# Kernel tuning notes

Hardware: AMD Instinct MI355X
Metric: run time of the kernel (lower is better)

The kernel has to match this reference:

```python
import jax, jax.numpy as jnp
import numpy as np

B, N, H = 128, 2048, 128
FEAT = 15


def setup_inputs() -> dict:
    key = jax.random.key(0)
    ks = jax.random.split(key, 24)
    f32 = jnp.float32
    inp = {
        'x':   jax.random.normal(ks[0], (B, N), f32),
        'x1':  jax.random.uniform(ks[1], (B, N), f32),
        'x2':  jax.random.uniform(ks[2], (B, N), f32),
        'z1':  jax.random.uniform(ks[3], (B, N), f32),
        'z2':  jax.random.uniform(ks[4], (B, N), f32),
        'x1E': jax.random.uniform(ks[5], (B, N), f32),
        'x2E': jax.random.uniform(ks[6], (B, N), f32),
        'z1E': jax.random.uniform(ks[7], (B, N), f32),
        'z2E': jax.random.uniform(ks[8], (B, N), f32),
        'muB': jax.random.uniform(ks[9], (B, 1), f32, 0.01, 0.1),
        'lb':  jax.random.normal(ks[10], (B, N), f32) - 2.0,
        'ub':  jax.random.normal(ks[11], (B, N), f32) + 2.0,
        'has_lb': jnp.ones((B, N), bool),
        'has_ub': jnp.ones((B, N), bool),
        # LSTM params (PyTorch gate order i, f, g, o)
        'W_ih': 0.1 * jax.random.normal(ks[12], (4 * H, FEAT), f32),
        'W_hh': 0.1 * jax.random.normal(ks[13], (4 * H, H), f32),
        'b_ih': 0.1 * jax.random.normal(ks[14], (4 * H,), f32),
        'b_hh': 0.1 * jax.random.normal(ks[15], (4 * H,), f32),
        # px_head: Linear(H,H) -> ReLU -> Linear(H,1)
        'W1': 0.1 * jax.random.normal(ks[16], (H, H), f32),
        'b1': 0.1 * jax.random.normal(ks[17], (H,), f32),
        'W2': 0.1 * jax.random.normal(ks[18], (1, H), f32),
        'b2': 0.1 * jax.random.normal(ks[19], (1,), f32),
    }
    return inp


def _forward(x, x1, x2, z1, z2, x1E, x2E, z1E, z2E, muB, lb, ub,
             W_ih, W_hh, b_ih, b_hh, W1, b1, W2, b2, has_lb, has_ub):
    Bb, n = x.shape
    eps = 1e-12
    # slack / bad-coordinate handling
    z1 = jnp.where((z1 + muB) <= 0, 0.0, z1)
    z2 = jnp.where((z2 + muB) <= 0, 0.0, z2)
    # quadratic merit stand-in: M = 0.5(||x||^2 + ||z1||^2 + ||z2||^2)
    grad_x, grad_z1, grad_z2 = x, z1, z2
    invD1 = jnp.clip((z1 + muB) / (x1 + muB + eps), 0.0, 100.0)
    invD2 = jnp.clip((z2 + muB) / (x2 + muB + eps), 0.0, 100.0)
    muB_bn = jnp.broadcast_to(muB, (Bb, n))
    # [B, n, 15] -> [B*n, 15]
    feat = jnp.stack([x, x1, x2, z1, z2, grad_x, grad_z1, grad_z2,
                      x1E, x2E, z1E, z2E, muB_bn, invD1, invD2], axis=-1)
    feat = feat.reshape(Bb * n, FEAT)
    # single-step LSTM cell, h0 = c0 = 0 so W_hh @ h0 vanishes
    gates = feat @ W_ih.T + b_ih + b_hh          # [B*n, 4H]
    i, f, g, o = jnp.split(gates, 4, axis=-1)
    c = jax.nn.sigmoid(i) * jnp.tanh(g)
    h = jax.nn.sigmoid(o) * jnp.tanh(c)          # [B*n, H]
    # MLP head -> per-coordinate positive step size
    p = jax.nn.relu(h @ W1.T + b1) @ W2.T + b2   # [B*n, 1]
    p_x = jnp.abs(p).reshape(Bb, n)
    # elementwise updates
    d_x = -p_x * grad_x
    x_new = x + d_x
    z1 = z1 - invD1 * (-p_x * grad_x + grad_z1)
    z2 = z2 - invD2 * (p_x * grad_x + grad_z2)
    x = x_new  # project_step = identity accept
    x1 = jnp.where(has_lb, x - lb, 0.0)
    x2 = jnp.where(has_ub, ub - x, 0.0)
    return jnp.concatenate([x, x1, x2, z1, z2], axis=-1)  # [B, 5n]


def reference(x, x1, x2, z1, z2, x1E, x2E, z1E, z2E, muB, lb, ub,
              has_lb, has_ub, W_ih, W_hh, b_ih, b_hh, W1, b1, W2, b2):
    return _forward(x, x1, x2, z1, z2, x1E, x2E, z1E, z2E, muB, lb, ub,
                    W_ih, W_hh, b_ih, b_hh, W1, b1, W2, b2, has_lb, has_ub)
```

## Files before the change

### kernel.cpp

```cpp
#include <hip/hip_runtime.h>


typedef _Float16 half8v  __attribute__((ext_vector_type(8)));
typedef _Float16 half4v  __attribute__((ext_vector_type(4)));
typedef float    float4v __attribute__((ext_vector_type(4)));

#define N_SZ   2048
#define ROWS   262144
#define BLOCKT 512
#define NWAVES 8
#define NBLK   512
#define WITERS 2
#define WROWS  32

#define HS 136
#define SS 40

__device__ __forceinline__ float fast_rcp(float x) { return __builtin_amdgcn_rcpf(x); }
__device__ __forceinline__ float sigm(float x)  { return fast_rcp(1.0f + __expf(-x)); }
__device__ __forceinline__ float tanh_f(float x){ return 1.0f - 2.0f * fast_rcp(1.0f + __expf(2.0f * x)); }
__device__ __forceinline__ float tanh_c(float y) {
    const float t = y * y;
    return y * __builtin_fmaf(t, __builtin_fmaf(t, __builtin_fmaf(t,
            -0.02714f, 0.12052f), -0.33157f), 0.99986f);
}

__global__ __launch_bounds__(BLOCKT)
void ps_lstm_hp2(const float* __restrict__ x_,
                 const float* __restrict__ x1_,
                 const float* __restrict__ x2_,
                 const float* __restrict__ z1_,
                 const float* __restrict__ z2_,
                 const float* __restrict__ x1E_,
                 const float* __restrict__ x2E_,
                 const float* __restrict__ z1E_,
                 const float* __restrict__ z2E_,
                 const float* __restrict__ muB_,
                 const float* __restrict__ lb_,
                 const float* __restrict__ ub_,
                 const float* __restrict__ Wih_,
                 const float* __restrict__ bih_,
                 const float* __restrict__ bhh_,
                 const float* __restrict__ W1_,
                 const float* __restrict__ b1_,
                 const float* __restrict__ W2_,
                 const float* __restrict__ b2_,
                 float* __restrict__ out_)
{
    __shared__ __align__(16) _Float16 fragWih[3 * 8 * 64 * 8];
    __shared__ __align__(16) _Float16 sW1T [128 * HS];
    __shared__ __align__(16) _Float16 sFeat[NWAVES][WROWS * 16];
    __shared__ __align__(16) _Float16 sHs  [NWAVES][16 * SS];
    __shared__ float sP[NWAVES][WROWS];

    const int tid  = threadIdx.x;
    const int lane = tid & 63;
    const int w    = tid >> 6;
    const int c    = lane & 15;
    const int q    = lane >> 4;

    for (int ch = tid; ch < 3 * 8 * 64; ch += BLOCKT) {
        const int g   = ch >> 9;
        const int rem = ch & 511;
        const int mt  = rem >> 6;
        const int l   = rem & 63;
        const int m   = mt * 16 + (l & 15);
        const int qq  = l >> 4;
        const int grow = (g == 0 ? m : (g == 1 ? 256 + m : 384 + m));
        half8v hh;
        #pragma unroll
        for (int j = 0; j < 8; ++j) {
            const int k = qq * 8 + j;
            float v = 0.0f;
            if (k < 15)       v = Wih_[grow * 15 + k];
            else if (k == 15) v = bih_[grow] + bhh_[grow];
            hh[j] = (_Float16)v;
        }
        *(half8v*)&fragWih[(size_t)ch * 8] = hh;
    }
    {
        const int n  = tid >> 2;
        const int q4 = tid & 3;
        const int k0 = q4 * 32;
        const float4* src = (const float4*)(W1_ + n * 128 + k0);
        #pragma unroll
        for (int v = 0; v < 4; ++v) {
            const float4 a  = src[2 * v];
            const float4 bq = src[2 * v + 1];
            half8v hh;
            hh[0] = (_Float16)a.x;  hh[1] = (_Float16)a.y;
            hh[2] = (_Float16)a.z;  hh[3] = (_Float16)a.w;
            hh[4] = (_Float16)bq.x; hh[5] = (_Float16)bq.y;
            hh[6] = (_Float16)bq.z; hh[7] = (_Float16)bq.w;
            *(half8v*)&sW1T[n * HS + k0 + v * 8] = hh;
        }
    }

    float b1r[8], w2r[8];
    #pragma unroll
    for (int nt = 0; nt < 8; ++nt) {
        b1r[nt] = b1_[nt * 16 + c];
        w2r[nt] = W2_[nt * 16 + c];
    }
    const float b2v = b2_[0];

    __syncthreads();

    const int gw = blockIdx.x * NWAVES + w;

    #pragma unroll 1
    for (int it = 0; it < WITERS; ++it) {
        const int rbase = (gw * WITERS + it) * WROWS;

        float ex = 0.f, ez1 = 0.f, ez2 = 0.f, eD1 = 0.f, eD2 = 0.f, elb = 0.f, eub = 0.f;
        if (lane < WROWS) {
            const int r = rbase + lane;
            const float x   = x_[r];
            const float x1  = x1_[r];
            const float x2  = x2_[r];
            float       z1  = z1_[r];
            float       z2  = z2_[r];
            const float x1E = x1E_[r];
            const float x2E = x2E_[r];
            const float z1E = z1E_[r];
            const float z2E = z2E_[r];
            const float mu  = muB_[r >> 11];

            z1 = ((z1 + mu) <= 0.0f) ? 0.0f : z1;
            z2 = ((z2 + mu) <= 0.0f) ? 0.0f : z2;
            float invD1 = (z1 + mu) * fast_rcp(x1 + mu + 1e-12f);
            float invD2 = (z2 + mu) * fast_rcp(x2 + mu + 1e-12f);
            invD1 = fminf(fmaxf(invD1, 0.0f), 100.0f);
            invD2 = fminf(fmaxf(invD2, 0.0f), 100.0f);

            const float f[15] = { x, x1, x2, z1, z2, x, z1, z2,
                                  x1E, x2E, z1E, z2E, mu, invD1, invD2 };
            half8v f0, f1;
            #pragma unroll
            for (int k = 0; k < 8; ++k) f0[k] = (_Float16)f[k];
            #pragma unroll
            for (int k = 0; k < 7; ++k) f1[k] = (_Float16)f[8 + k];
            f1[7] = (_Float16)1.0f;
            *(half8v*)&sFeat[w][lane * 16]     = f0;
            *(half8v*)&sFeat[w][lane * 16 + 8] = f1;

            ex = x; ez1 = z1; ez2 = z2; eD1 = invD1; eD2 = invD2;
            elb = lb_[r]; eub = ub_[r];
        }

        half8v z8;
        #pragma unroll
        for (int k = 0; k < 8; ++k) z8[k] = (_Float16)0.f;

        #pragma unroll 1
        for (int rh = 0; rh < 2; ++rh) {
            const half8v fB = (q < 2)
                ? *(const half8v*)&sFeat[w][(rh * 16 + c) * 16 + q * 8] : z8;

            float4v acc0 = {0.f,0.f,0.f,0.f}, acc1 = {0.f,0.f,0.f,0.f};
            float4v acc2 = {0.f,0.f,0.f,0.f}, acc3 = {0.f,0.f,0.f,0.f};
            float4v acc4 = {0.f,0.f,0.f,0.f}, acc5 = {0.f,0.f,0.f,0.f};
            float4v acc6 = {0.f,0.f,0.f,0.f}, acc7 = {0.f,0.f,0.f,0.f};

            #pragma unroll 1
            for (int kk = 0; kk < 4; ++kk) {
                #pragma unroll
                for (int mtl = 0; mtl < 2; ++mtl) {
                    const int mt = kk * 2 + mtl;
                    const half8v Ai = *(const half8v*)&fragWih[((0 * 8 + mt) * 64 + lane) * 8];
                    const half8v Ag = *(const half8v*)&fragWih[((1 * 8 + mt) * 64 + lane) * 8];
                    const half8v Ao = *(const half8v*)&fragWih[((2 * 8 + mt) * 64 + lane) * 8];
                    const float4v zc = {0.f, 0.f, 0.f, 0.f};
                    float4v di = __builtin_amdgcn_mfma_f32_16x16x32_f16(Ai, fB, zc, 0, 0, 0);
                    float4v dg = __builtin_amdgcn_mfma_f32_16x16x32_f16(Ag, fB, zc, 0, 0, 0);
                    float4v dv = __builtin_amdgcn_mfma_f32_16x16x32_f16(Ao, fB, zc, 0, 0, 0);
                    half4v h4;
                    #pragma unroll
                    for (int j = 0; j < 4; ++j) {
                        const float cv = sigm(di[j]) * tanh_f(dg[j]);
                        h4[j] = (_Float16)(sigm(dv[j]) * tanh_c(cv));
                    }
                    *(half4v*)&sHs[w][c * SS + mtl * 16 + q * 4] = h4;
                }
                const half8v hA = *(const half8v*)&sHs[w][c * SS + q * 8];
#define HEAD_STEP(NT, ACC) { \
                const half8v Bh = *(const half8v*)&sW1T[((NT) * 16 + c) * HS + kk * 32 + q * 8]; \
                ACC = __builtin_amdgcn_mfma_f32_16x16x32_f16(hA, Bh, ACC, 0, 0, 0); }
                HEAD_STEP(0, acc0)  HEAD_STEP(1, acc1)
                HEAD_STEP(2, acc2)  HEAD_STEP(3, acc3)
                HEAD_STEP(4, acc4)  HEAD_STEP(5, acc5)
                HEAD_STEP(6, acc6)  HEAD_STEP(7, acc7)
#undef HEAD_STEP
            }

            float p0 = 0.f, p1 = 0.f, p2 = 0.f, p3 = 0.f;
#define EPI(NT, ACC) { \
            const float bb = b1r[NT], ww = w2r[NT]; \
            p0 = __builtin_fmaf(fmaxf(ACC[0] + bb, 0.f), ww, p0); \
            p1 = __builtin_fmaf(fmaxf(ACC[1] + bb, 0.f), ww, p1); \
            p2 = __builtin_fmaf(fmaxf(ACC[2] + bb, 0.f), ww, p2); \
            p3 = __builtin_fmaf(fmaxf(ACC[3] + bb, 0.f), ww, p3); }
            EPI(0, acc0)  EPI(1, acc1)  EPI(2, acc2)  EPI(3, acc3)
            EPI(4, acc4)  EPI(5, acc5)  EPI(6, acc6)  EPI(7, acc7)
#undef EPI
            #pragma unroll
            for (int s = 1; s <= 8; s <<= 1) {
                p0 += __shfl_xor(p0, s, 64);
                p1 += __shfl_xor(p1, s, 64);
                p2 += __shfl_xor(p2, s, 64);
                p3 += __shfl_xor(p3, s, 64);
            }
            if (c == 0) {
                sP[w][rh * 16 + q * 4 + 0] = p0;
                sP[w][rh * 16 + q * 4 + 1] = p1;
                sP[w][rh * 16 + q * 4 + 2] = p2;
                sP[w][rh * 16 + q * 4 + 3] = p3;
            }
        }

        if (lane < WROWS) {
            const int   r     = rbase + lane;
            const int   b     = r >> 11;
            const int   n     = r & (N_SZ - 1);
            const float p     = sP[w][lane] + b2v;
            const float pxx   = fabsf(p) * ex;
            const float x_new = ex - pxx;
            float* ob = out_ + (size_t)b * (5 * N_SZ) + n;
            ob[0 * N_SZ] = x_new;
            ob[1 * N_SZ] = x_new - elb;
            ob[2 * N_SZ] = eub - x_new;
            ob[3 * N_SZ] = ez1 - eD1 * (ez1 - pxx);
            ob[4 * N_SZ] = ez2 - eD2 * (ez2 + pxx);
        }
    }
}

extern "C" void kernel_launch(void* const* d_in, const int* in_sizes, int n_in,
                              void* d_out, int out_size, void* d_ws, size_t ws_size,
                              hipStream_t stream) {
    (void)in_sizes; (void)n_in; (void)out_size; (void)d_ws; (void)ws_size;
    const float* x_   = (const float*)d_in[0];
    const float* x1_  = (const float*)d_in[1];
    const float* x2_  = (const float*)d_in[2];
    const float* z1_  = (const float*)d_in[3];
    const float* z2_  = (const float*)d_in[4];
    const float* x1E_ = (const float*)d_in[5];
    const float* x2E_ = (const float*)d_in[6];
    const float* z1E_ = (const float*)d_in[7];
    const float* z2E_ = (const float*)d_in[8];
    const float* muB_ = (const float*)d_in[9];
    const float* lb_  = (const float*)d_in[10];
    const float* ub_  = (const float*)d_in[11];
    const float* Wih_ = (const float*)d_in[14];
    const float* bih_ = (const float*)d_in[16];
    const float* bhh_ = (const float*)d_in[17];
    const float* W1_  = (const float*)d_in[18];
    const float* b1_  = (const float*)d_in[19];
    const float* W2_  = (const float*)d_in[20];
    const float* b2_  = (const float*)d_in[21];
    float* out_ = (float*)d_out;

    ps_lstm_hp2<<<NBLK, BLOCKT, 0, stream>>>(
        x_, x1_, x2_, z1_, z2_, x1E_, x2E_, z1E_, z2E_, muB_, lb_, ub_,
        Wih_, bih_, bhh_, W1_, b1_, W2_, b2_, out_);
}
```

Before: 141.7 us.

## Switch LSTM and head GEMMs to 16x16x16 MFMA, keeping h in registers

Replaces the 16x16x32 MFMA path with 16x16x16 f16 MFMAs. The K=16 input projection no longer wastes half the K dimension on zero padding. The gate output layout of one MFMA now matches the B-operand layout of the head MFMA, so the hidden state is passed in registers and the shared-memory staging buffer and its reads are removed. W1 is pre-swizzled into a per-lane fragment layout in LDS. This doubles the number of head MFMA instructions and loop trips, each with half the K.

```diff
diff --git a/kernel.cpp b/kernel.cpp
--- a/kernel.cpp
+++ b/kernel.cpp
@@ -12,9 +12,6 @@
 #define NBLK   512
 #define WITERS 2
 #define WROWS  32
-
-#define HS 136
-#define SS 40
 
 __device__ __forceinline__ float fast_rcp(float x) { return __builtin_amdgcn_rcpf(x); }
 __device__ __forceinline__ float sigm(float x)  { return fast_rcp(1.0f + __expf(-x)); }
@@ -26,7 +23,7 @@
 }
 
 __global__ __launch_bounds__(BLOCKT)
-void ps_lstm_hp2(const float* __restrict__ x_,
+void ps_lstm_k16(const float* __restrict__ x_,
                  const float* __restrict__ x1_,
                  const float* __restrict__ x2_,
                  const float* __restrict__ z1_,
@@ -47,10 +44,9 @@
                  const float* __restrict__ b2_,
                  float* __restrict__ out_)
 {
-    __shared__ __align__(16) _Float16 fragWih[3 * 8 * 64 * 8];
-    __shared__ __align__(16) _Float16 sW1T [128 * HS];
+    __shared__ __align__(16) _Float16 fragWih[3 * 8 * 64 * 4];
+    __shared__ __align__(16) _Float16 fragW1 [8 * 8 * 64 * 4];
     __shared__ __align__(16) _Float16 sFeat[NWAVES][WROWS * 16];
-    __shared__ __align__(16) _Float16 sHs  [NWAVES][16 * SS];
     __shared__ float sP[NWAVES][WROWS];
 
     const int tid  = threadIdx.x;
@@ -62,38 +58,32 @@
     for (int ch = tid; ch < 3 * 8 * 64; ch += BLOCKT) {
         const int g   = ch >> 9;
         const int rem = ch & 511;
-        const int mt  = rem >> 6;
+        const int kk  = rem >> 6;
         const int l   = rem & 63;
-        const int m   = mt * 16 + (l & 15);
-        const int qq  = l >> 4;
+        const int m   = kk * 16 + (l & 15);
+        const int q4  = l >> 4;
         const int grow = (g == 0 ? m : (g == 1 ? 256 + m : 384 + m));
-        half8v hh;
+        half4v hh;
         #pragma unroll
-        for (int j = 0; j < 8; ++j) {
-            const int k = qq * 8 + j;
-            float v = 0.0f;
-            if (k < 15)       v = Wih_[grow * 15 + k];
-            else if (k == 15) v = bih_[grow] + bhh_[grow];
+        for (int j = 0; j < 4; ++j) {
+            const int k = q4 * 4 + j;
+            const float v = (k < 15) ? Wih_[grow * 15 + k]
+                                     : (bih_[grow] + bhh_[grow]);
             hh[j] = (_Float16)v;
         }
-        *(half8v*)&fragWih[(size_t)ch * 8] = hh;
-    }
-    {
-        const int n  = tid >> 2;
-        const int q4 = tid & 3;
-        const int k0 = q4 * 32;
-        const float4* src = (const float4*)(W1_ + n * 128 + k0);
-        #pragma unroll
-        for (int v = 0; v < 4; ++v) {
-            const float4 a  = src[2 * v];
-            const float4 bq = src[2 * v + 1];
-            half8v hh;
-            hh[0] = (_Float16)a.x;  hh[1] = (_Float16)a.y;
-            hh[2] = (_Float16)a.z;  hh[3] = (_Float16)a.w;
-            hh[4] = (_Float16)bq.x; hh[5] = (_Float16)bq.y;
-            hh[6] = (_Float16)bq.z; hh[7] = (_Float16)bq.w;
-            *(half8v*)&sW1T[n * HS + k0 + v * 8] = hh;
-        }
+        *(half4v*)&fragWih[(size_t)ch * 4] = hh;
+    }
+    for (int ch = tid; ch < 8 * 8 * 64; ch += BLOCKT) {
+        const int nt = ch >> 9;
+        const int kk = (ch >> 6) & 7;
+        const int l  = ch & 63;
+        const int n2 = nt * 16 + (l & 15);
+        const int k0 = kk * 16 + (l >> 4) * 4;
+        const float4 a = *(const float4*)&W1_[n2 * 128 + k0];
+        half4v hh;
+        hh[0] = (_Float16)a.x; hh[1] = (_Float16)a.y;
+        hh[2] = (_Float16)a.z; hh[3] = (_Float16)a.w;
+        *(half4v*)&fragW1[(size_t)ch * 4] = hh;
     }
 
     float b1r[8], w2r[8];
@@ -148,14 +138,9 @@
             elb = lb_[r]; eub = ub_[r];
         }
 
-        half8v z8;
-        #pragma unroll
-        for (int k = 0; k < 8; ++k) z8[k] = (_Float16)0.f;
-
         #pragma unroll 1
         for (int rh = 0; rh < 2; ++rh) {
-            const half8v fB = (q < 2)
-                ? *(const half8v*)&sFeat[w][(rh * 16 + c) * 16 + q * 8] : z8;
+            const half4v fB = *(const half4v*)&sFeat[w][(rh * 16 + c) * 16 + q * 4];
 
             float4v acc0 = {0.f,0.f,0.f,0.f}, acc1 = {0.f,0.f,0.f,0.f};
             float4v acc2 = {0.f,0.f,0.f,0.f}, acc3 = {0.f,0.f,0.f,0.f};
@@ -163,34 +148,28 @@
             float4v acc6 = {0.f,0.f,0.f,0.f}, acc7 = {0.f,0.f,0.f,0.f};
 
             #pragma unroll 1
-            for (int kk = 0; kk < 4; ++kk) {
+            for (int kk = 0; kk < 8; ++kk) {
+                const half4v Ai = *(const half4v*)&fragWih[((0 * 8 + kk) * 64 + lane) * 4];
+                const half4v Ag = *(const half4v*)&fragWih[((1 * 8 + kk) * 64 + lane) * 4];
+                const half4v Ao = *(const half4v*)&fragWih[((2 * 8 + kk) * 64 + lane) * 4];
+                const float4v zc = {0.f, 0.f, 0.f, 0.f};
+                float4v di = __builtin_amdgcn_mfma_f32_16x16x16f16(Ai, fB, zc, 0, 0, 0);
+                float4v dg = __builtin_amdgcn_mfma_f32_16x16x16f16(Ag, fB, zc, 0, 0, 0);
+                float4v dv = __builtin_amdgcn_mfma_f32_16x16x16f16(Ao, fB, zc, 0, 0, 0);
+                half4v hB;
                 #pragma unroll
-                for (int mtl = 0; mtl < 2; ++mtl) {
-                    const int mt = kk * 2 + mtl;
-                    const half8v Ai = *(const half8v*)&fragWih[((0 * 8 + mt) * 64 + lane) * 8];
-                    const half8v Ag = *(const half8v*)&fragWih[((1 * 8 + mt) * 64 + lane) * 8];
-                    const half8v Ao = *(const half8v*)&fragWih[((2 * 8 + mt) * 64 + lane) * 8];
-                    const float4v zc = {0.f, 0.f, 0.f, 0.f};
-                    float4v di = __builtin_amdgcn_mfma_f32_16x16x32_f16(Ai, fB, zc, 0, 0, 0);
-                    float4v dg = __builtin_amdgcn_mfma_f32_16x16x32_f16(Ag, fB, zc, 0, 0, 0);
-                    float4v dv = __builtin_amdgcn_mfma_f32_16x16x32_f16(Ao, fB, zc, 0, 0, 0);
-                    half4v h4;
-                    #pragma unroll
-                    for (int j = 0; j < 4; ++j) {
-                        const float cv = sigm(di[j]) * tanh_f(dg[j]);
-                        h4[j] = (_Float16)(sigm(dv[j]) * tanh_c(cv));
-                    }
-                    *(half4v*)&sHs[w][c * SS + mtl * 16 + q * 4] = h4;
+                for (int j = 0; j < 4; ++j) {
+                    const float cv = sigm(di[j]) * tanh_f(dg[j]);
+                    hB[j] = (_Float16)(sigm(dv[j]) * tanh_c(cv));
                 }
-                const half8v hA = *(const half8v*)&sHs[w][c * SS + q * 8];
-#define HEAD_STEP(NT, ACC) { \
-                const half8v Bh = *(const half8v*)&sW1T[((NT) * 16 + c) * HS + kk * 32 + q * 8]; \
-                ACC = __builtin_amdgcn_mfma_f32_16x16x32_f16(hA, Bh, ACC, 0, 0, 0); }
-                HEAD_STEP(0, acc0)  HEAD_STEP(1, acc1)
-                HEAD_STEP(2, acc2)  HEAD_STEP(3, acc3)
-                HEAD_STEP(4, acc4)  HEAD_STEP(5, acc5)
-                HEAD_STEP(6, acc6)  HEAD_STEP(7, acc7)
-#undef HEAD_STEP
+#define HSTEP(NT, ACC) { \
+                const half4v Bw = *(const half4v*)&fragW1[(((NT) * 8 + kk) * 64 + lane) * 4]; \
+                ACC = __builtin_amdgcn_mfma_f32_16x16x16f16(hB, Bw, ACC, 0, 0, 0); }
+                HSTEP(0, acc0)  HSTEP(1, acc1)
+                HSTEP(2, acc2)  HSTEP(3, acc3)
+                HSTEP(4, acc4)  HSTEP(5, acc5)
+                HSTEP(6, acc6)  HSTEP(7, acc7)
+#undef HSTEP
             }
 
             float p0 = 0.f, p1 = 0.f, p2 = 0.f, p3 = 0.f;
@@ -260,7 +239,7 @@
     const float* b2_  = (const float*)d_in[21];
     float* out_ = (float*)d_out;
 
-    ps_lstm_hp2<<<NBLK, BLOCKT, 0, stream>>>(
+    ps_lstm_k16<<<NBLK, BLOCKT, 0, stream>>>(
         x_, x1_, x2_, z1_, z2_, x1E_, x2E_, z1E_, z2E_, muB_, lb_, ub_,
         Wih_, bih_, bhh_, W1_, b1_, W2_, b2_, out_);
 }
```

After: 140.6 us. Within noise of the previous version (-0.8%).
